# Kernel optimization log

Measured on AMD Instinct MI355X. Metric: run time of the kernel, lower is better.

The kernel has to match this reference:

```python
import jax, jax.numpy as jnp
import numpy as np

B, T, D, F, E, K, L, S = 8, 1024, 512, 1024, 8, 2, 2, 64
SE, SH = 64, 128  # subject_embed_dim, style_hidden_dim


def setup_inputs() -> dict:
    key = jax.random.key(0)
    ks = jax.random.split(key, 16)
    r = lambda i, shape, s=0.05: (jax.random.normal(ks[i], shape, jnp.float32) * s)
    return dict(
        x=jax.random.normal(ks[0], (B, T, D), jnp.float32),
        subject_ids=jax.random.randint(ks[1], (B,), 0, S),
        # per-layer LayerNorm params (L, D)
        ln_g=jnp.ones((L, D), jnp.float32), ln_b=jnp.zeros((L, D), jnp.float32),
        # per-layer SubjectStyleAlignment params (weights stored (in, out))
        subj_emb=r(2, (L, S, SE), 0.02),
        h1_w=r(3, (L, SE, SH)), h1_b=jnp.zeros((L, SH), jnp.float32),
        h2_w=r(4, (L, SH, SH)), h2_b=jnp.zeros((L, SH), jnp.float32),
        s1_w=r(5, (L, SH, SH // 2)), s1_b=jnp.zeros((L, SH // 2), jnp.float32),
        s2_w=r(6, (L, SH // 2, 2 * D)), s2_b=jnp.zeros((L, 2 * D), jnp.float32),
        # shared TopKRouter: Linear(D, D//2) -> ReLU -> Linear(D//2, E)
        g1_w=r(7, (D, D // 2)), g1_b=jnp.zeros((D // 2,), jnp.float32),
        g2_w=r(8, (D // 2, E)), g2_b=jnp.zeros((E,), jnp.float32),
        # shared ExpertPool of GLU experts (no bias)
        wi0=r(9, (E, D, F)), wi1=r(10, (E, D, F)), wo=r(11, (E, F, D)),
    )


def _layernorm(x, g, b):
    m = x.mean(-1, keepdims=True)
    v = x.var(-1, keepdims=True)  # biased, matches torch LayerNorm
    return (x - m) / jnp.sqrt(v + 1e-5) * g + b


def reference(x, subject_ids, ln_g, ln_b, subj_emb, h1_w, h1_b, h2_w, h2_b,
              s1_w, s1_b, s2_w, s2_b, g1_w, g1_b, g2_w, g2_b, wi0, wi1, wo):
    Bs, Ts, Ds = x.shape
    for l in range(L):  # small fixed layer loop; expert pool + router are shared
        res = x
        h = _layernorm(x, ln_g[l], ln_b[l])
        # SubjectStyleAlignment: instance norm over time axis per (B, D) channel
        mu = h.mean(1, keepdims=True)
        var = h.var(1, keepdims=True)
        hn = (h - mu) / jnp.sqrt(var + 1e-8)
        e = subj_emb[l][subject_ids]                               # (B, SE)
        hh = jax.nn.relu(e @ h1_w[l] + h1_b[l]) @ h2_w[l] + h2_b[l]
        sp = jax.nn.relu(hh @ s1_w[l] + s1_b[l]) @ s2_w[l] + s2_b[l]  # (B, 2D)
        gamma = jax.nn.softplus(sp[:, :Ds]) + 1e-8
        beta = sp[:, Ds:]
        h = hn * gamma[:, None, :] + beta[:, None, :]
        # Router (shared across layers)
        hf = h.reshape(-1, Ds)                                     # (N, D)
        logits = jax.nn.relu(hf @ g1_w + g1_b) @ g2_w + g2_b       # (N, E)
        probs = jax.nn.softmax(logits, -1)
        gates, idx = jax.lax.top_k(probs, K)                       # (N, K)
        gates = gates / (gates.sum(-1, keepdims=True) + 1e-8)
        # combine weights: cw[n, e] = sum_k gates[n,k] * [idx[n,k]==e]
        cw = (jax.nn.one_hot(idx, E, dtype=hf.dtype) * gates[..., None]).sum(1)  # (N, E)
        # GLU experts, computed dense over E then gated-combined
        hid = jax.nn.relu(jnp.einsum('nd,edf->enf', hf, wi0)) \
              * jnp.einsum('nd,edf->enf', hf, wi1)                 # (E, N, F)
        eo = jnp.einsum('enf,efd->end', hid, wo)                   # (E, N, D)
        y = jnp.einsum('ne,end->nd', cw, eo)                       # (N, D)
        x = res + y.reshape(Bs, Ts, Ds)
    return x
```

## Files before the change

kernel.cpp:

```cpp
#include <hip/hip_runtime.h>

typedef unsigned short u16;
typedef unsigned int   u32;
typedef _Float16       f16;
typedef __attribute__((ext_vector_type(8))) _Float16 f16x8;
typedef __attribute__((ext_vector_type(4))) float    f32x4;
typedef __attribute__((ext_vector_type(4))) double   dbl4;

#define NSLOT_ 16384

__device__ __forceinline__ u16 f16bits(f16 h){ union{f16 f; u16 u;} x; x.f = h; return x.u; }

__device__ __forceinline__ void gl_lds16(const void* gptr, void* lptr){
  __builtin_amdgcn_global_load_lds((const __attribute__((address_space(1))) u32*)gptr,
                                   (__attribute__((address_space(3))) u32*)lptr, 16, 0, 0);
}

__device__ __forceinline__ int roff(int row, int lks){
  return ((row >> 1) << 6) + ((lks ^ ((row >> 1) & 3)) << 4) + ((row & 1) << 3);
}

__global__ __launch_bounds__(256) void ln_kernel(const float* __restrict__ x,
    const float* __restrict__ g, const float* __restrict__ bb, float* __restrict__ h){
  int n = blockIdx.x, t = threadIdx.x;
  const float* xr = x + ((size_t)n << 9);
  float2 v = *(const float2*)&xr[t*2];
  double vx = v.x, vy = v.y;
  double s = vx + vy;
  double q = vx*vx + vy*vy;
  #pragma unroll
  for (int o = 32; o > 0; o >>= 1){ s += __shfl_down(s, o, 64); q += __shfl_down(q, o, 64); }
  __shared__ double ls[4], lq_[4];
  __shared__ double sm, sv;
  int wid = t >> 6, lane = t & 63;
  if (lane == 0){ ls[wid] = s; lq_[wid] = q; }
  __syncthreads();
  if (t == 0){
    double S = ls[0]+ls[1]+ls[2]+ls[3], Q = lq_[0]+lq_[1]+lq_[2]+lq_[3];
    double mean = S * (1.0/512.0);
    double var  = Q * (1.0/512.0) - mean*mean;
    sm = mean; sv = 1.0/sqrt(var + 1e-5);
  }
  __syncthreads();
  double mean = sm, inv = sv;
  int d = t*2;
  float2 o;
  o.x = (float)((vx - mean)*inv*(double)g[d]   + (double)bb[d]);
  o.y = (float)((vy - mean)*inv*(double)g[d+1] + (double)bb[d+1]);
  *(float2*)&h[((size_t)n<<9) + d] = o;
}

__global__ __launch_bounds__(256) void colstats(const float* __restrict__ h,
    double* __restrict__ cs, double* __restrict__ cq){
  int bid = blockIdx.x;
  int b = bid >> 3, ch = bid & 7;
  int t = threadIdx.x;
  int col = ch*64 + (t & 63);
  int tp = t >> 6;
  const float* base = h + ((size_t)b << 19);
  double s = 0.0, q = 0.0;
  for (int tt = tp; tt < 1024; tt += 4){
    double v = (double)base[((size_t)tt << 9) + col];
    s += v; q += v*v;
  }
  __shared__ double ls[4][64], lq[4][64];
  ls[tp][t & 63] = s; lq[tp][t & 63] = q;
  __syncthreads();
  if (tp == 0){
    double S = ls[0][t]+ls[1][t]+ls[2][t]+ls[3][t];
    double Q = lq[0][t]+lq[1][t]+lq[2][t]+lq[3][t];
    cs[(b<<9)+col] = S; cq[(b<<9)+col] = Q;
  }
}

__global__ __launch_bounds__(256) void subj_kernel(const int* __restrict__ sid,
    const float* __restrict__ semb,
    const float* __restrict__ h1w, const float* __restrict__ h1b,
    const float* __restrict__ h2w, const float* __restrict__ h2b,
    const float* __restrict__ s1w, const float* __restrict__ s1b,
    const float* __restrict__ s2w, const float* __restrict__ s2b,
    const double* __restrict__ cs, const double* __restrict__ cq,
    double* __restrict__ a64, double* __restrict__ c64, int l){
  __shared__ double ev[64], hid1[128], hh[128], sh[64], sp[1024];
  int t = threadIdx.x;
  int b = blockIdx.x;
  int s = sid[b];
  if (t < 64) ev[t] = (double)semb[l*4096 + s*64 + t];
  __syncthreads();
  if (t < 128){
    double acc = (double)h1b[l*128 + t];
    for (int i = 0; i < 64; ++i) acc += ev[i]*(double)h1w[l*8192 + i*128 + t];
    hid1[t] = acc > 0.0 ? acc : 0.0;
  }
  __syncthreads();
  if (t < 128){
    double acc = (double)h2b[l*128 + t];
    for (int i = 0; i < 128; ++i) acc += hid1[i]*(double)h2w[l*16384 + i*128 + t];
    hh[t] = acc;
  }
  __syncthreads();
  if (t < 64){
    double acc = (double)s1b[l*64 + t];
    for (int i = 0; i < 128; ++i) acc += hh[i]*(double)s1w[l*8192 + i*64 + t];
    sh[t] = acc > 0.0 ? acc : 0.0;
  }
  __syncthreads();
  for (int m = t; m < 1024; m += 256){
    double acc = (double)s2b[l*1024 + m];
    for (int j = 0; j < 64; ++j) acc += sh[j]*(double)s2w[l*65536 + j*1024 + m];
    sp[m] = acc;
  }
  __syncthreads();
  for (int d = t; d < 512; d += 256){
    double mu  = cs[(b<<9)+d] * (1.0/1024.0);
    double var = cq[(b<<9)+d] * (1.0/1024.0) - mu*mu;
    double inv = 1.0/sqrt(var + 1e-8);
    double spv = sp[d];
    double gamma = (spv > 30.0 ? spv : log1p(exp(spv))) + 1e-8;
    double beta  = sp[512 + d];
    double A = gamma * inv;
    a64[(b<<9)+d] = A;
    c64[(b<<9)+d] = beta - mu*A;
  }
}

__global__ __launch_bounds__(256) void hfcast(const float* __restrict__ h,
    const double* __restrict__ a64, const double* __restrict__ c64,
    u16* __restrict__ hfh, u16* __restrict__ hfl){
  size_t i0 = ((size_t)blockIdx.x*256 + threadIdx.x) * 8;
  int n = (int)(i0 >> 9);
  int d0 = (int)(i0 & 511);
  int b = n >> 10;
  float4 x0 = *(const float4*)&h[i0];
  float4 x1 = *(const float4*)&h[i0 + 4];
  dbl4 a0 = *(const dbl4*)&a64[(b<<9) + d0];
  dbl4 a1 = *(const dbl4*)&a64[(b<<9) + d0 + 4];
  dbl4 c0 = *(const dbl4*)&c64[(b<<9) + d0];
  dbl4 c1 = *(const dbl4*)&c64[(b<<9) + d0 + 4];
  float f[8];
  f[0] = (float)((double)x0.x*a0[0] + c0[0]);
  f[1] = (float)((double)x0.y*a0[1] + c0[1]);
  f[2] = (float)((double)x0.z*a0[2] + c0[2]);
  f[3] = (float)((double)x0.w*a0[3] + c0[3]);
  f[4] = (float)((double)x1.x*a1[0] + c1[0]);
  f[5] = (float)((double)x1.y*a1[1] + c1[1]);
  f[6] = (float)((double)x1.z*a1[2] + c1[2]);
  f[7] = (float)((double)x1.w*a1[3] + c1[3]);
  ushort4 oh0, oh1, ol0, ol1;
  u16 vh[8], vl[8];
  #pragma unroll
  for (int j = 0; j < 8; ++j){
    f16 hi = (f16)f[j];
    float rem = (f[j] - (float)hi) * 2048.f;
    f16 lo = (f16)rem;
    vh[j] = f16bits(hi); vl[j] = f16bits(lo);
  }
  oh0.x=vh[0]; oh0.y=vh[1]; oh0.z=vh[2]; oh0.w=vh[3];
  oh1.x=vh[4]; oh1.y=vh[5]; oh1.z=vh[6]; oh1.w=vh[7];
  ol0.x=vl[0]; ol0.y=vl[1]; ol0.z=vl[2]; ol0.w=vl[3];
  ol1.x=vl[4]; ol1.y=vl[5]; ol1.z=vl[6]; ol1.w=vl[7];
  *(ushort4*)&hfh[i0]   = oh0;
  *(ushort4*)&hfh[i0+4] = oh1;
  *(ushort4*)&hfl[i0]   = ol0;
  *(ushort4*)&hfl[i0+4] = ol1;
}

__global__ void zero_counts(int* __restrict__ counts){
  if (threadIdx.x < 8) counts[threadIdx.x] = 0;
}

__global__ __launch_bounds__(256) void gate2_kernel(const u16* __restrict__ hfh,
    const u16* __restrict__ hfl, const u16* __restrict__ g1Th, const u16* __restrict__ g1Tl,
    const float* __restrict__ g1b, const float* __restrict__ g2w, const float* __restrict__ g2b,
    int* __restrict__ idxo, float* __restrict__ wo_, int* __restrict__ counts){
  __shared__ double hid_s[16][258];
  __shared__ double lg[16*8];
  __shared__ int lcnt[8];
  int t = threadIdx.x, w = t >> 6, l = t & 63;
  int tok0 = blockIdx.x << 4;
  if (t < 8) lcnt[t] = 0;
  int lr = l & 15, lks = l >> 4;
  const u16* ahp = hfh + ((size_t)(tok0 + lr) << 9) + lks*8;
  const u16* alp = hfl + ((size_t)(tok0 + lr) << 9) + lks*8;
  const u16* bhp[4]; const u16* blp[4];
  #pragma unroll
  for (int nf = 0; nf < 4; ++nf){
    int col = w*64 + nf*16 + lr;
    bhp[nf] = g1Th + ((size_t)col << 9) + lks*8;
    blp[nf] = g1Tl + ((size_t)col << 9) + lks*8;
  }
  f32x4 hh[4], cr[4];
  #pragma unroll
  for (int nf = 0; nf < 4; ++nf)
    #pragma unroll
    for (int r = 0; r < 4; ++r){ hh[nf][r] = 0.f; cr[nf][r] = 0.f; }
  f16x8 ah = *(const f16x8*)ahp;
  f16x8 al = *(const f16x8*)alp;
  for (int kc = 0; kc < 512; kc += 32){
    int kn = (kc + 32) & 511;
    f16x8 ahn = *(const f16x8*)(ahp + kn);
    f16x8 aln = *(const f16x8*)(alp + kn);
    #pragma unroll
    for (int nf = 0; nf < 4; ++nf){
      f16x8 bh = *(const f16x8*)(bhp[nf] + kc);
      f16x8 bl = *(const f16x8*)(blp[nf] + kc);
      hh[nf] = __builtin_amdgcn_mfma_f32_16x16x32_f16(ah, bh, hh[nf], 0, 0, 0);
      cr[nf] = __builtin_amdgcn_mfma_f32_16x16x32_f16(ah, bl, cr[nf], 0, 0, 0);
      cr[nf] = __builtin_amdgcn_mfma_f32_16x16x32_f16(al, bh, cr[nf], 0, 0, 0);
    }
    ah = ahn; al = aln;
  }
  #pragma unroll
  for (int nf = 0; nf < 4; ++nf){
    int col = w*64 + nf*16 + lr;
    double gb = (double)g1b[col];
    #pragma unroll
    for (int r = 0; r < 4; ++r){
      int row = lks*4 + r;
      double v = (double)hh[nf][r] + (double)cr[nf][r]*(1.0/2048.0) + gb;
      hid_s[row][col] = v > 0.0 ? v : 0.0;
    }
  }
  __syncthreads();
  if (t < 128){
    int tok = t >> 3, e = t & 7;
    double la = (double)g2b[e];
    for (int k = 0; k < 256; ++k) la += hid_s[tok][k]*(double)g2w[(k<<3)+e];
    lg[(tok<<3)+e] = la;
  }
  __syncthreads();
  if (t < 16){
    double l0[8];
    #pragma unroll
    for (int e = 0; e < 8; ++e) l0[e] = lg[(t<<3)+e];
    double m = l0[0];
    #pragma unroll
    for (int e = 1; e < 8; ++e) m = fmax(m, l0[e]);
    double p[8]; double s = 0.0;
    #pragma unroll
    for (int e = 0; e < 8; ++e){ p[e] = exp(l0[e]-m); s += p[e]; }
    double b1 = -1e300, b2 = -1e300; int i1 = 0, i2 = 1;
    #pragma unroll
    for (int e = 0; e < 8; ++e){
      double v = l0[e];
      if (v > b1){ b2 = b1; i2 = i1; b1 = v; i1 = e; }
      else if (v > b2){ b2 = v; i2 = e; }
    }
    double pr1 = p[i1]/s, pr2 = p[i2]/s;
    double den = pr1 + pr2 + 1e-8;
    int n = tok0 + t;
    idxo[2*n] = i1; idxo[2*n+1] = i2;
    wo_[2*n] = (float)(pr1/den); wo_[2*n+1] = (float)(pr2/den);
    atomicAdd(&lcnt[i1], 1); atomicAdd(&lcnt[i2], 1);
  }
  __syncthreads();
  if (t < 8) atomicAdd(&counts[t], lcnt[t]);
}

__global__ void offsets_kernel(const int* __restrict__ counts, int* __restrict__ offs,
                               int* __restrict__ cur){
  if (threadIdx.x == 0 && blockIdx.x == 0){
    int run = 0;
    for (int e = 0; e < 8; ++e){ offs[e] = run; run += counts[e]; cur[e] = 0; }
  }
}

__global__ __launch_bounds__(256) void scatter_kernel(const int* __restrict__ idx,
    const int* __restrict__ offs, int* __restrict__ cur,
    int* __restrict__ tok_of, int* __restrict__ slot_of){
  __shared__ int lcnt[8], lbase[8];
  int t = threadIdx.x;
  int n = blockIdx.x*256 + t;
  if (t < 8) lcnt[t] = 0;
  __syncthreads();
  int e0 = idx[2*n], e1 = idx[2*n+1];
  int p0 = atomicAdd(&lcnt[e0], 1);
  int p1 = atomicAdd(&lcnt[e1], 1);
  __syncthreads();
  if (t < 8) lbase[t] = atomicAdd(&cur[t], lcnt[t]);
  __syncthreads();
  int s0 = offs[e0] + lbase[e0] + p0;
  int s1 = offs[e1] + lbase[e1] + p1;
  tok_of[s0] = n; tok_of[s1] = n;
  slot_of[2*n] = s0; slot_of[2*n+1] = s1;
}

__global__ __launch_bounds__(256) void cvtT16(const float* __restrict__ src,
    u16* __restrict__ dh, u16* __restrict__ dl, int R, int C){
  int bx = blockIdx.x;
  int tilesC = C >> 5, tilesR = R >> 5;
  int e = bx / (tilesR*tilesC);
  int rem = bx % (tilesR*tilesC);
  int rt = rem / tilesC, ct = rem % tilesC;
  __shared__ float tile[32][33];
  int t = threadIdx.x;
  int j = t & 31, i0 = t >> 5;
  const float* s = src + (size_t)e*R*C + (size_t)(rt*32)*C + ct*32;
  for (int ii = i0; ii < 32; ii += 8) tile[ii][j] = s[(size_t)ii*C + j];
  __syncthreads();
  size_t ob = (size_t)e*R*C + (size_t)(ct*32)*R + rt*32;
  for (int ii = i0; ii < 32; ii += 8){
    float v = tile[j][ii];
    f16 hi = (f16)v;
    float rem2 = (v - (float)hi) * 2048.f;
    f16 lo = (f16)rem2;
    dh[ob + (size_t)ii*R + j] = f16bits(hi);
    dl[ob + (size_t)ii*R + j] = f16bits(lo);
  }
}

__global__ __launch_bounds__(256) void up1_kernel(const u16* __restrict__ hfh,
    const u16* __restrict__ hfl,
    const u16* __restrict__ w0h, const u16* __restrict__ w0l,
    const u16* __restrict__ w1h, const u16* __restrict__ w1l,
    const int* __restrict__ tok_of, const int* __restrict__ offs, const int* __restrict__ counts,
    u16* __restrict__ hidh, u16* __restrict__ hidl){
  int bx = blockIdx.x;
  int e  = bx >> 11;
  int mt = (bx >> 4) & 127;
  int nt = bx & 15;
  int base = offs[e], cnt = counts[e];
  int row0 = mt << 7;
  if (row0 >= cnt) return;
  __shared__ __align__(16) u16 Ah[2][4096], Alo[2][4096];
  __shared__ __align__(16) u16 B0h[2][2048], B0l[2][2048], B1h[2][2048], B1l[2][2048];
  int t = threadIdx.x, w = t >> 6, l = t & 63;
  int wm = w >> 1, wn = w & 1;
  int lr = l & 15, lks = l >> 4;
  int riw = ((l >> 3) << 1) | (l & 1);
  int kc16s = ((((l >> 1) & 3) ^ ((l >> 3) & 3)) << 3);
  int ar1 = w*16 + riw;
  int tokA1, tokA2;
  { int ss = base + row0 + ar1;      ss = ss < NSLOT_ ? ss : NSLOT_-1; tokA1 = tok_of[ss]; }
  { int ss = base + row0 + 64 + ar1; ss = ss < NSLOT_ ? ss : NSLOT_-1; tokA2 = tok_of[ss]; }
  const u16* sAh1 = hfh + ((size_t)tokA1 << 9) + kc16s;
  const u16* sAh2 = hfh + ((size_t)tokA2 << 9) + kc16s;
  const u16* sAl1 = hfl + ((size_t)tokA1 << 9) + kc16s;
  const u16* sAl2 = hfl + ((size_t)tokA2 << 9) + kc16s;
  size_t bcol = (size_t)(e*1024 + nt*64);
  size_t bci = (bcol + (size_t)ar1) << 9;
  const u16* sB0h = w0h + bci + kc16s;
  const u16* sB0l = w0l + bci + kc16s;
  const u16* sB1h = w1h + bci + kc16s;
  const u16* sB1l = w1l + bci + kc16s;
  int aoff[4], boff[2];
  #pragma unroll
  for (int mi = 0; mi < 4; ++mi) aoff[mi] = roff(wm*64 + mi*16 + lr, lks);
  #pragma unroll
  for (int ni = 0; ni < 2; ++ni) boff[ni] = roff(wn*32 + ni*16 + lr, lks);
  f32x4 hh0[4][2], cr0[4][2], hh1[4][2], cr1[4][2];
  #pragma unroll
  for (int i = 0; i < 4; ++i)
    #pragma unroll
    for (int j = 0; j < 2; ++j)
      #pragma unroll
      for (int r = 0; r < 4; ++r){ hh0[i][j][r]=0.f; cr0[i][j][r]=0.f; hh1[i][j][r]=0.f; cr1[i][j][r]=0.f; }
#define STG_U(buf, kc) do{ \
    gl_lds16(sAh1 + (kc), &Ah[buf][t*8]); \
    gl_lds16(sAh2 + (kc), &Ah[buf][2048 + t*8]); \
    gl_lds16(sAl1 + (kc), &Alo[buf][t*8]); \
    gl_lds16(sAl2 + (kc), &Alo[buf][2048 + t*8]); \
    gl_lds16(sB0h + (kc), &B0h[buf][t*8]); \
    gl_lds16(sB0l + (kc), &B0l[buf][t*8]); \
    gl_lds16(sB1h + (kc), &B1h[buf][t*8]); \
    gl_lds16(sB1l + (kc), &B1l[buf][t*8]); }while(0)
  STG_U(0, 0);
  for (int ks = 0; ks < 16; ++ks){
    int cur = ks & 1;
    __syncthreads();
    if (ks < 15) STG_U(cur^1, (ks+1)*32);
    f16x8 ah[4], al[4], b0hv[2], b0lv[2], b1hv[2], b1lv[2];
    #pragma unroll
    for (int mi = 0; mi < 4; ++mi){
      ah[mi] = *(const f16x8*)&Ah[cur][aoff[mi]];
      al[mi] = *(const f16x8*)&Alo[cur][aoff[mi]];
    }
    #pragma unroll
    for (int ni = 0; ni < 2; ++ni){
      b0hv[ni] = *(const f16x8*)&B0h[cur][boff[ni]];
      b0lv[ni] = *(const f16x8*)&B0l[cur][boff[ni]];
      b1hv[ni] = *(const f16x8*)&B1h[cur][boff[ni]];
      b1lv[ni] = *(const f16x8*)&B1l[cur][boff[ni]];
    }
    #pragma unroll
    for (int mi = 0; mi < 4; ++mi)
      #pragma unroll
      for (int ni = 0; ni < 2; ++ni){
        hh0[mi][ni] = __builtin_amdgcn_mfma_f32_16x16x32_f16(ah[mi], b0hv[ni], hh0[mi][ni], 0, 0, 0);
        hh1[mi][ni] = __builtin_amdgcn_mfma_f32_16x16x32_f16(ah[mi], b1hv[ni], hh1[mi][ni], 0, 0, 0);
        cr0[mi][ni] = __builtin_amdgcn_mfma_f32_16x16x32_f16(ah[mi], b0lv[ni], cr0[mi][ni], 0, 0, 0);
        cr0[mi][ni] = __builtin_amdgcn_mfma_f32_16x16x32_f16(al[mi], b0hv[ni], cr0[mi][ni], 0, 0, 0);
        cr1[mi][ni] = __builtin_amdgcn_mfma_f32_16x16x32_f16(ah[mi], b1lv[ni], cr1[mi][ni], 0, 0, 0);
        cr1[mi][ni] = __builtin_amdgcn_mfma_f32_16x16x32_f16(al[mi], b1hv[ni], cr1[mi][ni], 0, 0, 0);
      }
  }
#undef STG_U
  #pragma unroll
  for (int mi = 0; mi < 4; ++mi){
    int rb = row0 + wm*64 + mi*16 + lks*4;
    #pragma unroll
    for (int r = 0; r < 4; ++r){
      int rr = rb + r;
      if (rr < cnt){
        size_t orow = ((size_t)(base + rr) << 10) + nt*64;
        #pragma unroll
        for (int ni = 0; ni < 2; ++ni){
          int col = wn*32 + ni*16 + lr;
          float u0 = hh0[mi][ni][r] + cr0[mi][ni][r]*(1.f/2048.f);
          float u1 = hh1[mi][ni][r] + cr1[mi][ni][r]*(1.f/2048.f);
          u0 = u0 > 0.f ? u0 : 0.f;
          float v = u0*u1;
          f16 vh = (f16)v;
          float rem = (v - (float)vh)*2048.f;
          hidh[orow + col] = f16bits(vh);
          hidl[orow + col] = f16bits((f16)rem);
        }
      }
    }
  }
}

__global__ __launch_bounds__(256) void down1_kernel(const u16* __restrict__ hidh,
    const u16* __restrict__ hidl, const u16* __restrict__ wdh, const u16* __restrict__ wdl,
    const int* __restrict__ offs, const int* __restrict__ counts, float* __restrict__ eo){
  int bx = blockIdx.x;
  int e  = bx >> 10;
  int mt = (bx >> 3) & 127;
  int nt = bx & 7;
  int base = offs[e], cnt = counts[e];
  int row0 = mt << 7;
  if (row0 >= cnt) return;
  __shared__ __align__(16) u16 Ah[2][4096], Alo[2][4096];
  __shared__ __align__(16) u16 Bh[2][2048], Bl[2][2048];
  int t = threadIdx.x, w = t >> 6, l = t & 63;
  int wm = w >> 1, wn = w & 1;
  int lr = l & 15, lks = l >> 4;
  int riw = ((l >> 3) << 1) | (l & 1);
  int kc16s = ((((l >> 1) & 3) ^ ((l >> 3) & 3)) << 3);
  int ar1 = w*16 + riw;
  int sA1c = base + row0 + ar1;      sA1c = sA1c < NSLOT_ ? sA1c : NSLOT_-1;
  int sA2c = base + row0 + 64 + ar1; sA2c = sA2c < NSLOT_ ? sA2c : NSLOT_-1;
  const u16* sAh1 = hidh + ((size_t)sA1c << 10) + kc16s;
  const u16* sAh2 = hidh + ((size_t)sA2c << 10) + kc16s;
  const u16* sAl1 = hidl + ((size_t)sA1c << 10) + kc16s;
  const u16* sAl2 = hidl + ((size_t)sA2c << 10) + kc16s;
  size_t bcol = (size_t)(e*512 + nt*64);
  size_t bci = (bcol + (size_t)ar1) << 10;
  const u16* sBh = wdh + bci + kc16s;
  const u16* sBl = wdl + bci + kc16s;
  int aoff[4], boff[2];
  #pragma unroll
  for (int mi = 0; mi < 4; ++mi) aoff[mi] = roff(wm*64 + mi*16 + lr, lks);
  #pragma unroll
  for (int ni = 0; ni < 2; ++ni) boff[ni] = roff(wn*32 + ni*16 + lr, lks);
  f32x4 hh[4][2], cr[4][2];
  #pragma unroll
  for (int i = 0; i < 4; ++i)
    #pragma unroll
    for (int j = 0; j < 2; ++j)
      #pragma unroll
      for (int r = 0; r < 4; ++r){ hh[i][j][r]=0.f; cr[i][j][r]=0.f; }
#define STG_D(buf, kc) do{ \
    gl_lds16(sAh1 + (kc), &Ah[buf][t*8]); \
    gl_lds16(sAh2 + (kc), &Ah[buf][2048 + t*8]); \
    gl_lds16(sAl1 + (kc), &Alo[buf][t*8]); \
    gl_lds16(sAl2 + (kc), &Alo[buf][2048 + t*8]); \
    gl_lds16(sBh + (kc), &Bh[buf][t*8]); \
    gl_lds16(sBl + (kc), &Bl[buf][t*8]); }while(0)
  STG_D(0, 0);
  for (int ks = 0; ks < 32; ++ks){
    int cur = ks & 1;
    __syncthreads();
    if (ks < 31) STG_D(cur^1, (ks+1)*32);
    f16x8 ah[4], al[4], bh[2], bl[2];
    #pragma unroll
    for (int mi = 0; mi < 4; ++mi){
      ah[mi] = *(const f16x8*)&Ah[cur][aoff[mi]];
      al[mi] = *(const f16x8*)&Alo[cur][aoff[mi]];
    }
    #pragma unroll
    for (int ni = 0; ni < 2; ++ni){
      bh[ni] = *(const f16x8*)&Bh[cur][boff[ni]];
      bl[ni] = *(const f16x8*)&Bl[cur][boff[ni]];
    }
    #pragma unroll
    for (int mi = 0; mi < 4; ++mi)
      #pragma unroll
      for (int ni = 0; ni < 2; ++ni){
        hh[mi][ni] = __builtin_amdgcn_mfma_f32_16x16x32_f16(ah[mi], bh[ni], hh[mi][ni], 0, 0, 0);
        cr[mi][ni] = __builtin_amdgcn_mfma_f32_16x16x32_f16(ah[mi], bl[ni], cr[mi][ni], 0, 0, 0);
        cr[mi][ni] = __builtin_amdgcn_mfma_f32_16x16x32_f16(al[mi], bh[ni], cr[mi][ni], 0, 0, 0);
      }
  }
#undef STG_D
  #pragma unroll
  for (int mi = 0; mi < 4; ++mi){
    int rb = row0 + wm*64 + mi*16 + lks*4;
    #pragma unroll
    for (int r = 0; r < 4; ++r){
      int rr = rb + r;
      if (rr < cnt){
        float* orow = eo + (((size_t)(base + rr)) << 9) + nt*64;
        #pragma unroll
        for (int ni = 0; ni < 2; ++ni)
          orow[wn*32 + ni*16 + lr] = hh[mi][ni][r] + cr[mi][ni][r]*(1.f/2048.f);
      }
    }
  }
}

__global__ __launch_bounds__(256) void uph_kernel(const u16* __restrict__ hfh,
    const u16* __restrict__ w0h, const u16* __restrict__ w1h,
    const int* __restrict__ tok_of, const int* __restrict__ offs, const int* __restrict__ counts,
    u16* __restrict__ hidh){
  int bx = blockIdx.x;
  int e  = bx >> 11;
  int mt = (bx >> 4) & 127;
  int nt = bx & 15;
  int base = offs[e], cnt = counts[e];
  int row0 = mt << 7;
  if (row0 >= cnt) return;
  __shared__ __align__(16) u16 Ah[2][4096];
  __shared__ __align__(16) u16 B0h[2][2048], B1h[2][2048];
  int t = threadIdx.x, w = t >> 6, l = t & 63;
  int wm = w >> 1, wn = w & 1;
  int lr = l & 15, lks = l >> 4;
  int riw = ((l >> 3) << 1) | (l & 1);
  int kc16s = ((((l >> 1) & 3) ^ ((l >> 3) & 3)) << 3);
  int ar1 = w*16 + riw;
  int tokA1, tokA2;
  { int ss = base + row0 + ar1;      ss = ss < NSLOT_ ? ss : NSLOT_-1; tokA1 = tok_of[ss]; }
  { int ss = base + row0 + 64 + ar1; ss = ss < NSLOT_ ? ss : NSLOT_-1; tokA2 = tok_of[ss]; }
  const u16* sAh1 = hfh + ((size_t)tokA1 << 9) + kc16s;
  const u16* sAh2 = hfh + ((size_t)tokA2 << 9) + kc16s;
  size_t bcol = (size_t)(e*1024 + nt*64);
  size_t bci = (bcol + (size_t)ar1) << 9;
  const u16* sB0 = w0h + bci + kc16s;
  const u16* sB1 = w1h + bci + kc16s;
  int aoff[4], boff[2];
  #pragma unroll
  for (int mi = 0; mi < 4; ++mi) aoff[mi] = roff(wm*64 + mi*16 + lr, lks);
  #pragma unroll
  for (int ni = 0; ni < 2; ++ni) boff[ni] = roff(wn*32 + ni*16 + lr, lks);
  f32x4 hh0[4][2], hh1[4][2];
  #pragma unroll
  for (int i = 0; i < 4; ++i)
    #pragma unroll
    for (int j = 0; j < 2; ++j)
      #pragma unroll
      for (int r = 0; r < 4; ++r){ hh0[i][j][r]=0.f; hh1[i][j][r]=0.f; }
#define STG_UH(buf, kc) do{ \
    gl_lds16(sAh1 + (kc), &Ah[buf][t*8]); \
    gl_lds16(sAh2 + (kc), &Ah[buf][2048 + t*8]); \
    gl_lds16(sB0 + (kc), &B0h[buf][t*8]); \
    gl_lds16(sB1 + (kc), &B1h[buf][t*8]); }while(0)
  STG_UH(0, 0);
  for (int ks = 0; ks < 16; ++ks){
    int cur = ks & 1;
    __syncthreads();
    if (ks < 15) STG_UH(cur^1, (ks+1)*32);
    f16x8 ah[4], b0v[2], b1v[2];
    #pragma unroll
    for (int mi = 0; mi < 4; ++mi) ah[mi] = *(const f16x8*)&Ah[cur][aoff[mi]];
    #pragma unroll
    for (int ni = 0; ni < 2; ++ni){
      b0v[ni] = *(const f16x8*)&B0h[cur][boff[ni]];
      b1v[ni] = *(const f16x8*)&B1h[cur][boff[ni]];
    }
    #pragma unroll
    for (int mi = 0; mi < 4; ++mi)
      #pragma unroll
      for (int ni = 0; ni < 2; ++ni){
        hh0[mi][ni] = __builtin_amdgcn_mfma_f32_16x16x32_f16(ah[mi], b0v[ni], hh0[mi][ni], 0, 0, 0);
        hh1[mi][ni] = __builtin_amdgcn_mfma_f32_16x16x32_f16(ah[mi], b1v[ni], hh1[mi][ni], 0, 0, 0);
      }
  }
#undef STG_UH
  #pragma unroll
  for (int mi = 0; mi < 4; ++mi){
    int rb = row0 + wm*64 + mi*16 + lks*4;
    #pragma unroll
    for (int r = 0; r < 4; ++r){
      int rr = rb + r;
      if (rr < cnt){
        size_t orow = ((size_t)(base + rr) << 10) + nt*64;
        #pragma unroll
        for (int ni = 0; ni < 2; ++ni){
          int col = wn*32 + ni*16 + lr;
          float u0 = hh0[mi][ni][r];
          u0 = u0 > 0.f ? u0 : 0.f;
          hidh[orow + col] = f16bits((f16)(u0*hh1[mi][ni][r]));
        }
      }
    }
  }
}

__global__ __launch_bounds__(256) void dnh_kernel(const u16* __restrict__ hidh,
    const u16* __restrict__ wdh,
    const int* __restrict__ offs, const int* __restrict__ counts, float* __restrict__ eo){
  int bx = blockIdx.x;
  int e  = bx >> 10;
  int mt = (bx >> 3) & 127;
  int nt = bx & 7;
  int base = offs[e], cnt = counts[e];
  int row0 = mt << 7;
  if (row0 >= cnt) return;
  __shared__ __align__(16) u16 Ah[2][4096];
  __shared__ __align__(16) u16 Bh[2][2048];
  int t = threadIdx.x, w = t >> 6, l = t & 63;
  int wm = w >> 1, wn = w & 1;
  int lr = l & 15, lks = l >> 4;
  int riw = ((l >> 3) << 1) | (l & 1);
  int kc16s = ((((l >> 1) & 3) ^ ((l >> 3) & 3)) << 3);
  int ar1 = w*16 + riw;
  int sA1c = base + row0 + ar1;      sA1c = sA1c < NSLOT_ ? sA1c : NSLOT_-1;
  int sA2c = base + row0 + 64 + ar1; sA2c = sA2c < NSLOT_ ? sA2c : NSLOT_-1;
  const u16* sAh1 = hidh + ((size_t)sA1c << 10) + kc16s;
  const u16* sAh2 = hidh + ((size_t)sA2c << 10) + kc16s;
  size_t bcol = (size_t)(e*512 + nt*64);
  const u16* sB = wdh + ((bcol + (size_t)ar1) << 10) + kc16s;
  int aoff[4], boff[2];
  #pragma unroll
  for (int mi = 0; mi < 4; ++mi) aoff[mi] = roff(wm*64 + mi*16 + lr, lks);
  #pragma unroll
  for (int ni = 0; ni < 2; ++ni) boff[ni] = roff(wn*32 + ni*16 + lr, lks);
  f32x4 hh[4][2];
  #pragma unroll
  for (int i = 0; i < 4; ++i)
    #pragma unroll
    for (int j = 0; j < 2; ++j)
      #pragma unroll
      for (int r = 0; r < 4; ++r) hh[i][j][r] = 0.f;
#define STG_DH(buf, kc) do{ \
    gl_lds16(sAh1 + (kc), &Ah[buf][t*8]); \
    gl_lds16(sAh2 + (kc), &Ah[buf][2048 + t*8]); \
    gl_lds16(sB + (kc), &Bh[buf][t*8]); }while(0)
  STG_DH(0, 0);
  for (int ks = 0; ks < 32; ++ks){
    int cur = ks & 1;
    __syncthreads();
    if (ks < 31) STG_DH(cur^1, (ks+1)*32);
    f16x8 ah[4], bh[2];
    #pragma unroll
    for (int mi = 0; mi < 4; ++mi) ah[mi] = *(const f16x8*)&Ah[cur][aoff[mi]];
    #pragma unroll
    for (int ni = 0; ni < 2; ++ni) bh[ni] = *(const f16x8*)&Bh[cur][boff[ni]];
    #pragma unroll
    for (int mi = 0; mi < 4; ++mi)
      #pragma unroll
      for (int ni = 0; ni < 2; ++ni)
        hh[mi][ni] = __builtin_amdgcn_mfma_f32_16x16x32_f16(ah[mi], bh[ni], hh[mi][ni], 0, 0, 0);
  }
#undef STG_DH
  #pragma unroll
  for (int mi = 0; mi < 4; ++mi){
    int rb = row0 + wm*64 + mi*16 + lks*4;
    #pragma unroll
    for (int r = 0; r < 4; ++r){
      int rr = rb + r;
      if (rr < cnt){
        float* orow = eo + (((size_t)(base + rr)) << 9) + nt*64;
        #pragma unroll
        for (int ni = 0; ni < 2; ++ni)
          orow[wn*32 + ni*16 + lr] = hh[mi][ni][r];
      }
    }
  }
}

__global__ __launch_bounds__(128) void gather_kernel(const float* __restrict__ xin,
    const float* __restrict__ eo, const int* __restrict__ slot_of, const float* __restrict__ wv,
    float* __restrict__ out){
  int n = blockIdx.x, t = threadIdx.x;
  int s0 = slot_of[2*n], s1 = slot_of[2*n+1];
  double w0 = wv[2*n], w1 = wv[2*n+1];
  float4 xi = *(const float4*)&xin[((size_t)n << 9) + t*4];
  float4 e0 = *(const float4*)&eo[((size_t)s0 << 9) + t*4];
  float4 e1 = *(const float4*)&eo[((size_t)s1 << 9) + t*4];
  float4 o;
  o.x = (float)((double)xi.x + w0*(double)e0.x + w1*(double)e1.x);
  o.y = (float)((double)xi.y + w0*(double)e0.y + w1*(double)e1.y);
  o.z = (float)((double)xi.z + w0*(double)e0.z + w1*(double)e1.z);
  o.w = (float)((double)xi.w + w0*(double)e0.w + w1*(double)e1.w);
  *(float4*)&out[((size_t)n << 9) + t*4] = o;
}

extern "C" void kernel_launch(void* const* d_in, const int* in_sizes, int n_in,
                              void* d_out, int out_size, void* d_ws, size_t ws_size,
                              hipStream_t stream) {
  (void)in_sizes; (void)n_in; (void)out_size; (void)ws_size;
  const float* x0   = (const float*)d_in[0];
  const int*   sid  = (const int*)  d_in[1];
  const float* ln_g = (const float*)d_in[2];
  const float* ln_b = (const float*)d_in[3];
  const float* semb = (const float*)d_in[4];
  const float* h1w  = (const float*)d_in[5];
  const float* h1b  = (const float*)d_in[6];
  const float* h2w  = (const float*)d_in[7];
  const float* h2b  = (const float*)d_in[8];
  const float* s1w  = (const float*)d_in[9];
  const float* s1b  = (const float*)d_in[10];
  const float* s2w  = (const float*)d_in[11];
  const float* s2b  = (const float*)d_in[12];
  const float* g1w  = (const float*)d_in[13];
  const float* g1b  = (const float*)d_in[14];
  const float* g2w  = (const float*)d_in[15];
  const float* g2b  = (const float*)d_in[16];
  const float* wi0  = (const float*)d_in[17];
  const float* wi1  = (const float*)d_in[18];
  const float* wo   = (const float*)d_in[19];

  char* W = (char*)d_ws;
  float*  h      = (float*)(W + 0);
  u16*    hfh    = (u16*)  (W + 16777216ULL);
  u16*    hfl    = (u16*)  (W + 25165824ULL);
  float*  eo32   = (float*)(W + 0);
  u16*    hid16h = (u16*)  (W + 33554432ULL);
  u16*    hid16l = (u16*)  (W + 67108864ULL);
  u16*    w0Th   = (u16*)  (W + 100663296ULL);
  u16*    w0Tl   = (u16*)  (W + 109051904ULL);
  u16*    w1Th   = (u16*)  (W + 117440512ULL);
  u16*    w1Tl   = (u16*)  (W + 125829120ULL);
  u16*    woTh   = (u16*)  (W + 134217728ULL);
  u16*    woTl   = (u16*)  (W + 142606336ULL);
  u16*    g1Th   = (u16*)  (W + 150994944ULL);
  u16*    g1Tl   = (u16*)  (W + 151257088ULL);
  double* cs     = (double*)(W + 151519232ULL);
  double* cq     = (double*)(W + 151552000ULL);
  double* a64    = (double*)(W + 151584768ULL);
  double* c64    = (double*)(W + 151617536ULL);
  int*    idxa   = (int*)   (W + 151650304ULL);
  float*  warr   = (float*) (W + 151715840ULL);
  int*    tok_of = (int*)   (W + 151781376ULL);
  int*    slot_of= (int*)   (W + 151846912ULL);
  int*    counts = (int*)   (W + 151912448ULL);
  int*    cur    = counts + 8;
  int*    offs   = counts + 16;

  cvtT16<<<4096, 256, 0, stream>>>(wi0, w0Th, w0Tl, 512, 1024);
  cvtT16<<<4096, 256, 0, stream>>>(wi1, w1Th, w1Tl, 512, 1024);
  cvtT16<<<4096, 256, 0, stream>>>(wo,  woTh, woTl, 1024, 512);
  cvtT16<<<128,  256, 0, stream>>>(g1w, g1Th, g1Tl, 512, 256);

  for (int l = 0; l < 2; ++l){
    const float* xin = l ? (const float*)d_out : x0;
    ln_kernel<<<8192, 256, 0, stream>>>(xin, ln_g + l*512, ln_b + l*512, h);
    colstats<<<64, 256, 0, stream>>>(h, cs, cq);
    subj_kernel<<<8, 256, 0, stream>>>(sid, semb, h1w, h1b, h2w, h2b, s1w, s1b, s2w, s2b,
                                       cs, cq, a64, c64, l);
    hfcast<<<2048, 256, 0, stream>>>(h, a64, c64, hfh, hfl);
    zero_counts<<<1, 64, 0, stream>>>(counts);
    gate2_kernel<<<512, 256, 0, stream>>>(hfh, hfl, g1Th, g1Tl, g1b, g2w, g2b, idxa, warr, counts);
    offsets_kernel<<<1, 1, 0, stream>>>(counts, offs, cur);
    scatter_kernel<<<32, 256, 0, stream>>>(idxa, offs, cur, tok_of, slot_of);
    if (l == 0){
      up1_kernel<<<16384, 256, 0, stream>>>(hfh, hfl, w0Th, w0Tl, w1Th, w1Tl,
                                            tok_of, offs, counts, hid16h, hid16l);
      down1_kernel<<<8192, 256, 0, stream>>>(hid16h, hid16l, woTh, woTl, offs, counts, eo32);
    } else {
      uph_kernel<<<16384, 256, 0, stream>>>(hfh, w0Th, w1Th, tok_of, offs, counts, hid16h);
      dnh_kernel<<<8192, 256, 0, stream>>>(hid16h, woTh, offs, counts, eo32);
    }
    gather_kernel<<<8192, 128, 0, stream>>>(xin, eo32, slot_of, warr, (float*)d_out);
  }
}
```

Measured before the change: 868.7 us.

## Fuse layer-0 gather with layer-1 LayerNorm and interleave expert block order

Unrolls the two-layer loop and adds a gather_ln kernel that writes the layer-0 residual output and computes the layer-1 LayerNorm in the same pass, removing one full read of the activations and one launch. eo32 moves to its own workspace region so it no longer aliases h. The expert GEMM kernels now take the expert index from the low bits of the block index, so experts are interleaved across the grid instead of contiguous, which is meant to spread active blocks evenly and skip empty tiles more uniformly. This uses more workspace and changes the L2 reuse pattern of the weights.

```diff
diff --git a/kernel.cpp b/kernel.cpp
--- a/kernel.cpp
+++ b/kernel.cpp
@@ -48,6 +48,49 @@
   o.x = (float)((vx - mean)*inv*(double)g[d]   + (double)bb[d]);
   o.y = (float)((vy - mean)*inv*(double)g[d+1] + (double)bb[d+1]);
   *(float2*)&h[((size_t)n<<9) + d] = o;
+}
+
+__global__ __launch_bounds__(128) void gather_ln(const float* __restrict__ xin,
+    const float* __restrict__ eo, const int* __restrict__ slot_of, const float* __restrict__ wv,
+    const float* __restrict__ g, const float* __restrict__ bb,
+    float* __restrict__ out, float* __restrict__ h){
+  int n = blockIdx.x, t = threadIdx.x;
+  int s0 = slot_of[2*n], s1 = slot_of[2*n+1];
+  double w0 = wv[2*n], w1 = wv[2*n+1];
+  float4 xi = *(const float4*)&xin[((size_t)n << 9) + t*4];
+  float4 e0 = *(const float4*)&eo[((size_t)s0 << 9) + t*4];
+  float4 e1 = *(const float4*)&eo[((size_t)s1 << 9) + t*4];
+  double o0 = (double)xi.x + w0*(double)e0.x + w1*(double)e1.x;
+  double o1 = (double)xi.y + w0*(double)e0.y + w1*(double)e1.y;
+  double o2 = (double)xi.z + w0*(double)e0.z + w1*(double)e1.z;
+  double o3 = (double)xi.w + w0*(double)e0.w + w1*(double)e1.w;
+  float4 o; o.x = (float)o0; o.y = (float)o1; o.z = (float)o2; o.w = (float)o3;
+  *(float4*)&out[((size_t)n << 9) + t*4] = o;
+  double vx = o.x, vy = o.y, vz = o.z, vw = o.w;
+  double s = vx+vy+vz+vw;
+  double q = vx*vx+vy*vy+vz*vz+vw*vw;
+  #pragma unroll
+  for (int off = 32; off > 0; off >>= 1){ s += __shfl_down(s, off, 64); q += __shfl_down(q, off, 64); }
+  __shared__ double ls[2], lq_[2];
+  __shared__ double sm, sv;
+  int wid = t >> 6, lane = t & 63;
+  if (lane == 0){ ls[wid] = s; lq_[wid] = q; }
+  __syncthreads();
+  if (t == 0){
+    double S = ls[0]+ls[1], Q = lq_[0]+lq_[1];
+    double mean = S * (1.0/512.0);
+    double var  = Q * (1.0/512.0) - mean*mean;
+    sm = mean; sv = 1.0/sqrt(var + 1e-5);
+  }
+  __syncthreads();
+  double mean = sm, inv = sv;
+  int d = t*4;
+  float4 ho;
+  ho.x = (float)((vx - mean)*inv*(double)g[d]   + (double)bb[d]);
+  ho.y = (float)((vy - mean)*inv*(double)g[d+1] + (double)bb[d+1]);
+  ho.z = (float)((vz - mean)*inv*(double)g[d+2] + (double)bb[d+2]);
+  ho.w = (float)((vw - mean)*inv*(double)g[d+3] + (double)bb[d+3]);
+  *(float4*)&h[((size_t)n<<9) + d] = ho;
 }
 
 __global__ __launch_bounds__(256) void colstats(const float* __restrict__ h,
@@ -316,9 +359,10 @@
     const int* __restrict__ tok_of, const int* __restrict__ offs, const int* __restrict__ counts,
     u16* __restrict__ hidh, u16* __restrict__ hidl){
   int bx = blockIdx.x;
-  int e  = bx >> 11;
-  int mt = (bx >> 4) & 127;
-  int nt = bx & 15;
+  int e  = bx & 7;
+  int q  = bx >> 3;
+  int mt = q >> 4;
+  int nt = q & 15;
   int base = offs[e], cnt = counts[e];
   int row0 = mt << 7;
   if (row0 >= cnt) return;
@@ -424,9 +468,10 @@
     const u16* __restrict__ hidl, const u16* __restrict__ wdh, const u16* __restrict__ wdl,
     const int* __restrict__ offs, const int* __restrict__ counts, float* __restrict__ eo){
   int bx = blockIdx.x;
-  int e  = bx >> 10;
-  int mt = (bx >> 3) & 127;
-  int nt = bx & 7;
+  int e  = bx & 7;
+  int q  = bx >> 3;
+  int mt = q >> 3;
+  int nt = q & 7;
   int base = offs[e], cnt = counts[e];
   int row0 = mt << 7;
   if (row0 >= cnt) return;
@@ -514,9 +559,10 @@
     const int* __restrict__ tok_of, const int* __restrict__ offs, const int* __restrict__ counts,
     u16* __restrict__ hidh){
   int bx = blockIdx.x;
-  int e  = bx >> 11;
-  int mt = (bx >> 4) & 127;
-  int nt = bx & 15;
+  int e  = bx & 7;
+  int q  = bx >> 3;
+  int mt = q >> 4;
+  int nt = q & 15;
   int base = offs[e], cnt = counts[e];
   int row0 = mt << 7;
   if (row0 >= cnt) return;
@@ -600,9 +646,10 @@
     const u16* __restrict__ wdh,
     const int* __restrict__ offs, const int* __restrict__ counts, float* __restrict__ eo){
   int bx = blockIdx.x;
-  int e  = bx >> 10;
-  int mt = (bx >> 3) & 127;
-  int nt = bx & 7;
+  int e  = bx & 7;
+  int q  = bx >> 3;
+  int mt = q >> 3;
+  int nt = q & 7;
   int base = offs[e], cnt = counts[e];
   int row0 = mt << 7;
   if (row0 >= cnt) return;
@@ -715,7 +762,7 @@
   float*  h      = (float*)(W + 0);
   u16*    hfh    = (u16*)  (W + 16777216ULL);
   u16*    hfl    = (u16*)  (W + 25165824ULL);
-  float*  eo32   = (float*)(W + 0);
+  float*  eo32   = (float*)(W + 167772160ULL);
   u16*    hid16h = (u16*)  (W + 33554432ULL);
   u16*    hid16l = (u16*)  (W + 67108864ULL);
   u16*    w0Th   = (u16*)  (W + 100663296ULL);
@@ -743,25 +790,29 @@
   cvtT16<<<4096, 256, 0, stream>>>(wo,  woTh, woTl, 1024, 512);
   cvtT16<<<128,  256, 0, stream>>>(g1w, g1Th, g1Tl, 512, 256);
 
-  for (int l = 0; l < 2; ++l){
-    const float* xin = l ? (const float*)d_out : x0;
-    ln_kernel<<<8192, 256, 0, stream>>>(xin, ln_g + l*512, ln_b + l*512, h);
-    colstats<<<64, 256, 0, stream>>>(h, cs, cq);
-    subj_kernel<<<8, 256, 0, stream>>>(sid, semb, h1w, h1b, h2w, h2b, s1w, s1b, s2w, s2b,
-                                       cs, cq, a64, c64, l);
-    hfcast<<<2048, 256, 0, stream>>>(h, a64, c64, hfh, hfl);
-    zero_counts<<<1, 64, 0, stream>>>(counts);
-    gate2_kernel<<<512, 256, 0, stream>>>(hfh, hfl, g1Th, g1Tl, g1b, g2w, g2b, idxa, warr, counts);
-    offsets_kernel<<<1, 1, 0, stream>>>(counts, offs, cur);
-    scatter_kernel<<<32, 256, 0, stream>>>(idxa, offs, cur, tok_of, slot_of);
-    if (l == 0){
-      up1_kernel<<<16384, 256, 0, stream>>>(hfh, hfl, w0Th, w0Tl, w1Th, w1Tl,
-                                            tok_of, offs, counts, hid16h, hid16l);
-      down1_kernel<<<8192, 256, 0, stream>>>(hid16h, hid16l, woTh, woTl, offs, counts, eo32);
-    } else {
-      uph_kernel<<<16384, 256, 0, stream>>>(hfh, w0Th, w1Th, tok_of, offs, counts, hid16h);
-      dnh_kernel<<<8192, 256, 0, stream>>>(hid16h, woTh, offs, counts, eo32);
-    }
-    gather_kernel<<<8192, 128, 0, stream>>>(xin, eo32, slot_of, warr, (float*)d_out);
-  }
-}
+  ln_kernel<<<8192, 256, 0, stream>>>(x0, ln_g, ln_b, h);
+  colstats<<<64, 256, 0, stream>>>(h, cs, cq);
+  subj_kernel<<<8, 256, 0, stream>>>(sid, semb, h1w, h1b, h2w, h2b, s1w, s1b, s2w, s2b,
+                                     cs, cq, a64, c64, 0);
+  hfcast<<<2048, 256, 0, stream>>>(h, a64, c64, hfh, hfl);
+  zero_counts<<<1, 64, 0, stream>>>(counts);
+  gate2_kernel<<<512, 256, 0, stream>>>(hfh, hfl, g1Th, g1Tl, g1b, g2w, g2b, idxa, warr, counts);
+  offsets_kernel<<<1, 1, 0, stream>>>(counts, offs, cur);
+  scatter_kernel<<<32, 256, 0, stream>>>(idxa, offs, cur, tok_of, slot_of);
+  up1_kernel<<<16384, 256, 0, stream>>>(hfh, hfl, w0Th, w0Tl, w1Th, w1Tl,
+                                        tok_of, offs, counts, hid16h, hid16l);
+  down1_kernel<<<8192, 256, 0, stream>>>(hid16h, hid16l, woTh, woTl, offs, counts, eo32);
+  gather_ln<<<8192, 128, 0, stream>>>(x0, eo32, slot_of, warr, ln_g + 512, ln_b + 512,
+                                      (float*)d_out, h);
+  colstats<<<64, 256, 0, stream>>>(h, cs, cq);
+  subj_kernel<<<8, 256, 0, stream>>>(sid, semb, h1w, h1b, h2w, h2b, s1w, s1b, s2w, s2b,
+                                     cs, cq, a64, c64, 1);
+  hfcast<<<2048, 256, 0, stream>>>(h, a64, c64, hfh, hfl);
+  zero_counts<<<1, 64, 0, stream>>>(counts);
+  gate2_kernel<<<512, 256, 0, stream>>>(hfh, hfl, g1Th, g1Tl, g1b, g2w, g2b, idxa, warr, counts);
+  offsets_kernel<<<1, 1, 0, stream>>>(counts, offs, cur);
+  scatter_kernel<<<32, 256, 0, stream>>>(idxa, offs, cur, tok_of, slot_of);
+  uph_kernel<<<16384, 256, 0, stream>>>(hfh, w0Th, w1Th, tok_of, offs, counts, hid16h);
+  dnh_kernel<<<8192, 256, 0, stream>>>(hid16h, woTh, offs, counts, eo32);
+  gather_kernel<<<8192, 128, 0, stream>>>((const float*)d_out, eo32, slot_of, warr, (float*)d_out);
+}
```

Measured after the change: 1.101 ms. 1.27x slower.
